# Kernel optimization log

Hardware: AMD Instinct MI355X
Metric: run time of the kernel (lower is better)

## Reference

```python
import jax, jax.numpy as jnp
import numpy as np

ALPHA = 3.0
MIN_DIFF = 0.1
N = 8192


def setup_inputs() -> dict:
    key = jax.random.key(0)
    k1, k2 = jax.random.split(key)
    pred = jax.random.normal(k1, (N, 1), dtype=jnp.float32)
    target = jax.random.normal(k2, (N, 1), dtype=jnp.float32)
    return {"pred": pred, "target": target}


def reference(pred, target):
    pred = pred.reshape(-1)
    target = target.reshape(-1)
    n = pred.shape[0]

    regression_loss = jnp.mean((pred - target) ** 2)

    # all upper-triangular (i < j) pairs, as in torch.triu_indices(N, N, 1)
    rows, cols = jnp.triu_indices(n, k=1)  # each has n*(n-1)/2 entries

    diff_target = target[rows] - target[cols]
    confidence = jax.lax.stop_gradient(jnp.abs(diff_target))
    mask = confidence > MIN_DIFF
    sgn = jnp.sign(jax.lax.stop_gradient(diff_target))

    bpr_diff = jax.nn.log_sigmoid((pred[rows] - pred[cols]) * sgn)
    pairwise_loss = -confidence * bpr_diff

    cnt = jnp.sum(mask)
    pairwise_mean = jnp.sum(jnp.where(mask, pairwise_loss, 0.0)) / jnp.maximum(cnt, 1).astype(pairwise_loss.dtype)

    return jnp.where(cnt > 0, regression_loss + ALPHA * pairwise_mean, regression_loss)
```

## Files before the change

### kernel.cpp

```cpp
#include <hip/hip_runtime.h>
#include <math.h>

#define NN 8192
#define TS 128
#define NT (NN / TS)
#define NTILES ((NT * (NT + 1)) / 2)
#define BLOCK 256
#define ALPHA_C 3.0f
#define MIN_DIFF_C 0.1f

__global__ __launch_bounds__(BLOCK, 8) void pair_kernel(
    const float* __restrict__ pred, const float* __restrict__ targ,
    float4* __restrict__ parts) {
    const int b = blockIdx.x;
    int ti = (int)((2.0 * NT + 1.0 -
                    sqrt((2.0 * NT + 1.0) * (2.0 * NT + 1.0) - 8.0 * (double)b)) * 0.5);
    int start = ti * NT - (ti * (ti - 1)) / 2;
    if (b < start) { --ti; start = ti * NT - (ti * (ti - 1)) / 2; }
    else if (b >= start + (NT - ti)) { start += NT - ti; ++ti; }
    const int tj = ti + (b - start);

    __shared__ float2 sT[TS];
    const int tid  = threadIdx.x;
    const int jl   = tid & (TS - 1);
    const int half = tid >> 7;
    const int i0   = ti * TS;
    const int j    = tj * TS + jl;

    if (tid < TS) sT[tid] = make_float2(pred[i0 + tid], targ[i0 + tid]);
    __syncthreads();

    const float pj  = pred[j];
    const float tjv = targ[j];

    float s = 0.0f;
    float c = 0.0f;
    float r = 0.0f;

    const int ib = half * (TS / 2);
    const int ie = ib + (TS / 2);

    if (ti < tj) {
        #pragma unroll 8
        for (int ii = ib; ii < ie; ++ii) {
            const float2 v  = sT[ii];
            const float dt  = v.y - tjv;
            const float dp  = v.x - pj;
            const bool valid = fabsf(dt) > MIN_DIFF_C;
            const unsigned sb = __float_as_uint(dt) & 0x80000000u;
            const float x   = __uint_as_float(__float_as_uint(dp) ^ sb);
            const float nax = __uint_as_float(__float_as_uint(x) | 0x80000000u);
            const float l = fmaxf(-x, 0.0f) + __logf(1.0f + __expf(nax));
            const float cm = valid ? fabsf(dt) : 0.0f;
            s = fmaf(cm, l, s);
            c += valid ? 1.0f : 0.0f;
        }
    } else {
        #pragma unroll 4
        for (int ii = ib; ii < ie; ++ii) {
            const float2 v  = sT[ii];
            const int   i   = i0 + ii;
            const float dt  = v.y - tjv;
            const float dp  = v.x - pj;
            const bool valid = (i < j) && (fabsf(dt) > MIN_DIFF_C);
            const unsigned sb = __float_as_uint(dt) & 0x80000000u;
            const float x   = __uint_as_float(__float_as_uint(dp) ^ sb);
            const float nax = __uint_as_float(__float_as_uint(x) | 0x80000000u);
            const float l = fmaxf(-x, 0.0f) + __logf(1.0f + __expf(nax));
            const float cm = valid ? fabsf(dt) : 0.0f;
            s = fmaf(cm, l, s);
            c += valid ? 1.0f : 0.0f;
        }
        if (half == 0) { const float d = pj - tjv; r = d * d; }
    }

    #pragma unroll
    for (int off = 32; off > 0; off >>= 1) {
        s += __shfl_down(s, off, 64);
        c += __shfl_down(c, off, 64);
        r += __shfl_down(r, off, 64);
    }
    __shared__ float red_s[4], red_c[4], red_r[4];
    const int wave = tid >> 6;
    const int lane = tid & 63;
    if (lane == 0) { red_s[wave] = s; red_c[wave] = c; red_r[wave] = r; }
    __syncthreads();
    if (tid == 0) {
        parts[b] = make_float4(red_s[0] + red_s[1] + red_s[2] + red_s[3],
                               red_c[0] + red_c[1] + red_c[2] + red_c[3],
                               red_r[0] + red_r[1] + red_r[2] + red_r[3], 0.0f);
    }
}

__global__ __launch_bounds__(256) void finalize_kernel(
    const float4* __restrict__ parts, float* __restrict__ out) {
    float s = 0.0f, c = 0.0f, r = 0.0f;
    for (int t = threadIdx.x; t < NTILES; t += 256) {
        const float4 v = parts[t];
        s += v.x; c += v.y; r += v.z;
    }
    #pragma unroll
    for (int off = 32; off > 0; off >>= 1) {
        s += __shfl_down(s, off, 64);
        c += __shfl_down(c, off, 64);
        r += __shfl_down(r, off, 64);
    }
    __shared__ float red_s[4], red_c[4], red_r[4];
    const int wave = threadIdx.x >> 6;
    const int lane = threadIdx.x & 63;
    if (lane == 0) { red_s[wave] = s; red_c[wave] = c; red_r[wave] = r; }
    __syncthreads();
    if (threadIdx.x == 0) {
        const float fs = red_s[0] + red_s[1] + red_s[2] + red_s[3];
        const float fc = red_c[0] + red_c[1] + red_c[2] + red_c[3];
        const float fr = red_r[0] + red_r[1] + red_r[2] + red_r[3];
        const float reg = fr / (float)NN;
        out[0] = (fc > 0.0f) ? (reg + ALPHA_C * (fs / fmaxf(fc, 1.0f))) : reg;
    }
}

extern "C" void kernel_launch(void* const* d_in, const int* in_sizes, int n_in,
                              void* d_out, int out_size, void* d_ws, size_t ws_size,
                              hipStream_t stream) {
    const float* pred = (const float*)d_in[0];
    const float* targ = (const float*)d_in[1];
    float* out = (float*)d_out;
    float4* parts = (float4*)d_ws;

    pair_kernel<<<NTILES, BLOCK, 0, stream>>>(pred, targ, parts);
    finalize_kernel<<<1, 256, 0, stream>>>(parts, out);
}
```

Before: 86.08 us.

## Retile pair kernel and compute softplus in base-2 with hardware exp2/log

```diff
diff --git a/kernel.cpp b/kernel.cpp
--- a/kernel.cpp
+++ b/kernel.cpp
@@ -2,76 +2,82 @@
 #include <math.h>
 
 #define NN 8192
-#define TS 128
-#define NT (NN / TS)
-#define NTILES ((NT * (NT + 1)) / 2)
-#define BLOCK 256
+#define JT 256
+#define IC 64
+#define NJT (NN / JT)
+#define NBLOCKS (2 * NJT * (NJT + 1))
 #define ALPHA_C 3.0f
 #define MIN_DIFF_C 0.1f
+#define LOG2E 1.44269504088896340736f
+#define LN2   0.69314718055994530942f
 
-__global__ __launch_bounds__(BLOCK, 8) void pair_kernel(
+__global__ __launch_bounds__(256, 8) void pair_kernel(
     const float* __restrict__ pred, const float* __restrict__ targ,
     float4* __restrict__ parts) {
     const int b = blockIdx.x;
-    int ti = (int)((2.0 * NT + 1.0 -
-                    sqrt((2.0 * NT + 1.0) * (2.0 * NT + 1.0) - 8.0 * (double)b)) * 0.5);
-    int start = ti * NT - (ti * (ti - 1)) / 2;
-    if (b < start) { --ti; start = ti * NT - (ti * (ti - 1)) / 2; }
-    else if (b >= start + (NT - ti)) { start += NT - ti; ++ti; }
-    const int tj = ti + (b - start);
+    int t = (int)((sqrt(1.0 + 2.0 * (double)b) - 1.0) * 0.5);
+    while (2 * (t + 1) * (t + 2) <= b) ++t;
+    while (2 * t * (t + 1) > b) --t;
+    const int ic = b - 2 * t * (t + 1);
+    const int j0 = t * JT;
+    const int i0 = ic * IC;
 
-    __shared__ float2 sT[TS];
-    const int tid  = threadIdx.x;
-    const int jl   = tid & (TS - 1);
-    const int half = tid >> 7;
-    const int i0   = ti * TS;
-    const int j    = tj * TS + jl;
-
-    if (tid < TS) sT[tid] = make_float2(pred[i0 + tid], targ[i0 + tid]);
-    __syncthreads();
-
-    const float pj  = pred[j];
-    const float tjv = targ[j];
+    const int tid = threadIdx.x;
+    const int j = j0 + tid;
+    const float pj   = pred[j];
+    const float tjv  = targ[j];
+    const float npjl = -pj * LOG2E;
 
     float s = 0.0f;
     float c = 0.0f;
     float r = 0.0f;
 
-    const int ib = half * (TS / 2);
-    const int ie = ib + (TS / 2);
+    const bool diag = (ic >= 4 * t);
 
-    if (ti < tj) {
-        #pragma unroll 8
-        for (int ii = ib; ii < ie; ++ii) {
-            const float2 v  = sT[ii];
-            const float dt  = v.y - tjv;
-            const float dp  = v.x - pj;
-            const bool valid = fabsf(dt) > MIN_DIFF_C;
-            const unsigned sb = __float_as_uint(dt) & 0x80000000u;
-            const float x   = __uint_as_float(__float_as_uint(dp) ^ sb);
-            const float nax = __uint_as_float(__float_as_uint(x) | 0x80000000u);
-            const float l = fmaxf(-x, 0.0f) + __logf(1.0f + __expf(nax));
-            const float cm = valid ? fabsf(dt) : 0.0f;
-            s = fmaf(cm, l, s);
-            c += valid ? 1.0f : 0.0f;
+    if (!diag) {
+        #pragma unroll
+        for (int ch = 0; ch < IC / 8; ++ch) {
+            const float4 pa = *(const float4*)(pred + i0 + ch * 8);
+            const float4 pb = *(const float4*)(pred + i0 + ch * 8 + 4);
+            const float4 ta = *(const float4*)(targ + i0 + ch * 8);
+            const float4 tb = *(const float4*)(targ + i0 + ch * 8 + 4);
+            const float pi[8] = {pa.x, pa.y, pa.z, pa.w, pb.x, pb.y, pb.z, pb.w};
+            const float ti[8] = {ta.x, ta.y, ta.z, ta.w, tb.x, tb.y, tb.z, tb.w};
+            #pragma unroll
+            for (int k = 0; k < 8; ++k) {
+                const float dt  = ti[k] - tjv;
+                const float dps = fmaf(pi[k], LOG2E, npjl);
+                const float ny  = (dt < 0.0f) ? dps : -dps;
+                const float e   = __builtin_amdgcn_exp2f(ny);
+                const float lg  = __builtin_amdgcn_logf(1.0f + e);
+                const bool valid = fabsf(dt) > MIN_DIFF_C;
+                s = fmaf(valid ? fabsf(dt) : 0.0f, lg, s);
+                c += valid ? 1.0f : 0.0f;
+            }
         }
     } else {
-        #pragma unroll 4
-        for (int ii = ib; ii < ie; ++ii) {
-            const float2 v  = sT[ii];
-            const int   i   = i0 + ii;
-            const float dt  = v.y - tjv;
-            const float dp  = v.x - pj;
-            const bool valid = (i < j) && (fabsf(dt) > MIN_DIFF_C);
-            const unsigned sb = __float_as_uint(dt) & 0x80000000u;
-            const float x   = __uint_as_float(__float_as_uint(dp) ^ sb);
-            const float nax = __uint_as_float(__float_as_uint(x) | 0x80000000u);
-            const float l = fmaxf(-x, 0.0f) + __logf(1.0f + __expf(nax));
-            const float cm = valid ? fabsf(dt) : 0.0f;
-            s = fmaf(cm, l, s);
-            c += valid ? 1.0f : 0.0f;
+        #pragma unroll
+        for (int ch = 0; ch < IC / 8; ++ch) {
+            const float4 pa = *(const float4*)(pred + i0 + ch * 8);
+            const float4 pb = *(const float4*)(pred + i0 + ch * 8 + 4);
+            const float4 ta = *(const float4*)(targ + i0 + ch * 8);
+            const float4 tb = *(const float4*)(targ + i0 + ch * 8 + 4);
+            const float pi[8] = {pa.x, pa.y, pa.z, pa.w, pb.x, pb.y, pb.z, pb.w};
+            const float ti[8] = {ta.x, ta.y, ta.z, ta.w, tb.x, tb.y, tb.z, tb.w};
+            #pragma unroll
+            for (int k = 0; k < 8; ++k) {
+                const int i = i0 + ch * 8 + k;
+                const float dt  = ti[k] - tjv;
+                const float dps = fmaf(pi[k], LOG2E, npjl);
+                const float ny  = (dt < 0.0f) ? dps : -dps;
+                const float e   = __builtin_amdgcn_exp2f(ny);
+                const float lg  = __builtin_amdgcn_logf(1.0f + e);
+                const bool valid = (i < j) && (fabsf(dt) > MIN_DIFF_C);
+                s = fmaf(valid ? fabsf(dt) : 0.0f, lg, s);
+                c += valid ? 1.0f : 0.0f;
+            }
         }
-        if (half == 0) { const float d = pj - tjv; r = d * d; }
+        if (ic == 4 * t + 3) { const float d = pj - tjv; r = d * d; }
     }
 
     #pragma unroll
@@ -95,8 +101,8 @@
 __global__ __launch_bounds__(256) void finalize_kernel(
     const float4* __restrict__ parts, float* __restrict__ out) {
     float s = 0.0f, c = 0.0f, r = 0.0f;
-    for (int t = threadIdx.x; t < NTILES; t += 256) {
-        const float4 v = parts[t];
+    for (int i = threadIdx.x; i < NBLOCKS; i += 256) {
+        const float4 v = parts[i];
         s += v.x; c += v.y; r += v.z;
     }
     #pragma unroll
@@ -115,7 +121,8 @@
         const float fc = red_c[0] + red_c[1] + red_c[2] + red_c[3];
         const float fr = red_r[0] + red_r[1] + red_r[2] + red_r[3];
         const float reg = fr / (float)NN;
-        out[0] = (fc > 0.0f) ? (reg + ALPHA_C * (fs / fmaxf(fc, 1.0f))) : reg;
+        const float pm  = LN2 * fs / fmaxf(fc, 1.0f);
+        out[0] = (fc > 0.0f) ? (reg + ALPHA_C * pm) : reg;
     }
 }
 
@@ -127,6 +134,6 @@
     float* out = (float*)d_out;
     float4* parts = (float4*)d_ws;
 
-    pair_kernel<<<NTILES, BLOCK, 0, stream>>>(pred, targ, parts);
+    pair_kernel<<<NBLOCKS, 256, 0, stream>>>(pred, targ, parts);
     finalize_kernel<<<1, 256, 0, stream>>>(parts, out);
 }
```

Result: slower. 148.2 us (+72.2%).
